# Kernel tuning notes

Hardware: AMD Instinct MI355X
Metric: run time of the kernel (lower is better)

The kernel has to match this reference:

```python
import jax, jax.numpy as jnp
import numpy as np

D_MODEL = 128
N_HEADS = 4
HEAD_DIM = D_MODEL // N_HEADS


def setup_inputs() -> dict:
    key = jax.random.key(0)
    ks = jax.random.split(key, 16)
    s = 0.05
    B, N, T = 1, 1024, 1024
    return {
        "node_states": jax.random.normal(ks[0], (B, N, D_MODEL), jnp.float32),
        "task_features": jax.random.normal(ks[1], (T, D_MODEL), jnp.float32),
        "in_proj_w": jax.random.normal(ks[2], (3 * D_MODEL, D_MODEL), jnp.float32) * s,
        "in_proj_b": jnp.zeros((3 * D_MODEL,), jnp.float32),
        "out_w": jax.random.normal(ks[3], (D_MODEL, D_MODEL), jnp.float32) * s,
        "out_b": jnp.zeros((D_MODEL,), jnp.float32),
        "W1": jax.random.normal(ks[4], (256, 256), jnp.float32) * s,
        "b1": jnp.zeros((256,), jnp.float32),
        "W2": jax.random.normal(ks[5], (128, 256), jnp.float32) * s,
        "b2": jnp.zeros((128,), jnp.float32),
        "W3": jax.random.normal(ks[6], (1, 128), jnp.float32) * s,
        "b3": jnp.zeros((1,), jnp.float32),
        "Wc1": jax.random.normal(ks[7], (256, D_MODEL), jnp.float32) * s,
        "bc1": jnp.zeros((256,), jnp.float32),
        "Wc2": jax.random.normal(ks[8], (32, 256), jnp.float32) * s,
        "bc2": jnp.zeros((32,), jnp.float32),
    }


def _mha(x, in_proj_w, in_proj_b, out_w, out_b):
    # x: [B, N, D]; torch nn.MultiheadAttention self-attention, batch_first.
    B, N, D = x.shape
    q = x @ in_proj_w[:D].T + in_proj_b[:D]
    k = x @ in_proj_w[D:2 * D].T + in_proj_b[D:2 * D]
    v = x @ in_proj_w[2 * D:].T + in_proj_b[2 * D:]
    def split(t):  # [B,N,D] -> [B,H,N,dh]
        return t.reshape(B, N, N_HEADS, HEAD_DIM).transpose(0, 2, 1, 3)
    qh, kh, vh = split(q), split(k), split(v)
    scores = jnp.einsum("bhqd,bhkd->bhqk", qh, kh) / jnp.sqrt(jnp.float32(HEAD_DIM))
    attn = jax.nn.softmax(scores, axis=-1)  # [B,H,N,N]
    ctx = jnp.einsum("bhqk,bhkd->bhqd", attn, vh)
    ctx = ctx.transpose(0, 2, 1, 3).reshape(B, N, D)
    out = ctx @ out_w.T + out_b
    attn_avg = attn.mean(axis=1)  # torch averages heads by default -> [B,N,N]
    return out, attn_avg


def reference(node_states, task_features, in_proj_w, in_proj_b, out_w, out_b,
              W1, b1, W2, b2, W3, b3, Wc1, bc1, Wc2, bc2):
    attended, attn_w = _mha(node_states, in_proj_w, in_proj_b, out_w, out_b)
    nodes = attended[0]  # original loop only uses batch 0: [N, D]
    # Linear on concat([task, node]) == split-weight sum; vectorize pairwise.
    t1 = task_features @ W1[:, :D_MODEL].T          # [T, 256]
    n1 = nodes @ W1[:, D_MODEL:].T                  # [N, 256]
    h1 = jax.nn.relu(t1[:, None, :] + n1[None, :, :] + b1)      # [T, N, 256]
    h2 = jax.nn.relu(jnp.einsum("tnc,kc->tnk", h1, W2) + b2)   # [T, N, 128]
    matching_scores = jax.nn.sigmoid(jnp.einsum("tnk,ok->tn", h2, W3) + b3[0])
    global_state = attended.mean(axis=1)            # [B, D]
    coordination_logits = jax.nn.relu(global_state @ Wc1.T + bc1) @ Wc2.T + bc2
    return matching_scores, coordination_logits, attn_w
```

## Files before the change

### kernel.cpp

```cpp
#include <hip/hip_runtime.h>
#include <hip/hip_fp16.h>
#include <stdint.h>


typedef __attribute__((ext_vector_type(4))) float floatx4;
typedef __attribute__((ext_vector_type(8))) _Float16 half8;

#define OFF_QKV  0x000000u
#define OFF_T1H  0x280000u
#define OFF_N1H  0x300000u
#define OFF_W2F  0x380000u
#define OFF_GS   0x398000u
#define OFF_SM   0x3A0000u
#define OFF_SL   0x3A8000u
#define OFF_SC   0x400000u
#define OFF_CTP  0xC00000u

__device__ __forceinline__ unsigned pkadd(unsigned a, unsigned b) {
    unsigned r; asm("v_pk_add_f16 %0, %1, %2" : "=v"(r) : "v"(a), "v"(b)); return r;
}
__device__ __forceinline__ unsigned pkmax(unsigned a, unsigned b) {
    unsigned r; asm("v_pk_max_f16 %0, %1, %2" : "=v"(r) : "v"(a), "v"(b)); return r;
}
__device__ __forceinline__ unsigned pk2h(float a, float b) {
    return (unsigned)__half_as_ushort(__float2half(a)) |
           ((unsigned)__half_as_ushort(__float2half(b)) << 16);
}
__device__ __forceinline__ float h2f(unsigned short u) {
    return __half2float(__ushort_as_half(u));
}

template<bool BIAS, bool F16OUT>
__device__ __forceinline__ void gemm_dev(
    const float* __restrict__ A, int lda,
    const float* __restrict__ B, int ldb,
    const float* __restrict__ bias,
    void* __restrict__ Cv, int ldc, int K, float scale,
    int m0, int n0, float (*As)[64], float (*Bs)[64])
{
    const int tid = threadIdx.x;
    const int tx = tid & 15, ty = tid >> 4;
    const int lr = tid >> 2;
    const int lk = (tid & 3) * 4;
    float c[4][4] = {};

    for (int k0 = 0; k0 < K; k0 += 16) {
        float4 a  = *(const float4*)&A[(long)(m0 + lr) * lda + k0 + lk];
        float4 bb = *(const float4*)&B[(long)(n0 + lr) * ldb + k0 + lk];
        __syncthreads();
        As[lk + 0][lr] = a.x;  As[lk + 1][lr] = a.y;  As[lk + 2][lr] = a.z;  As[lk + 3][lr] = a.w;
        Bs[lk + 0][lr] = bb.x; Bs[lk + 1][lr] = bb.y; Bs[lk + 2][lr] = bb.z; Bs[lk + 3][lr] = bb.w;
        __syncthreads();
#pragma unroll
        for (int k = 0; k < 16; k++) {
            float4 av = *(const float4*)&As[k][ty * 4];
            float4 bv = *(const float4*)&Bs[k][tx * 4];
            c[0][0] += av.x * bv.x; c[0][1] += av.x * bv.y; c[0][2] += av.x * bv.z; c[0][3] += av.x * bv.w;
            c[1][0] += av.y * bv.x; c[1][1] += av.y * bv.y; c[1][2] += av.y * bv.z; c[1][3] += av.y * bv.w;
            c[2][0] += av.z * bv.x; c[2][1] += av.z * bv.y; c[2][2] += av.z * bv.z; c[2][3] += av.z * bv.w;
            c[3][0] += av.w * bv.x; c[3][1] += av.w * bv.y; c[3][2] += av.w * bv.z; c[3][3] += av.w * bv.w;
        }
    }

    float bsv[4] = {0.f, 0.f, 0.f, 0.f};
    if (BIAS) {
        float4 t = *(const float4*)&bias[n0 + tx * 4];
        bsv[0] = t.x; bsv[1] = t.y; bsv[2] = t.z; bsv[3] = t.w;
    }
#pragma unroll
    for (int i = 0; i < 4; i++) {
        float v0 = c[i][0] * scale + bsv[0];
        float v1 = c[i][1] * scale + bsv[1];
        float v2 = c[i][2] * scale + bsv[2];
        float v3 = c[i][3] * scale + bsv[3];
        long m = m0 + ty * 4 + i;
        if (F16OUT) {
            unsigned short* Cp = (unsigned short*)Cv;
            ushort4 o;
            o.x = __half_as_ushort(__float2half(v0));
            o.y = __half_as_ushort(__float2half(v1));
            o.z = __half_as_ushort(__float2half(v2));
            o.w = __half_as_ushort(__float2half(v3));
            *(ushort4*)&Cp[m * ldc + n0 + tx * 4] = o;
        } else {
            float* Cp = (float*)Cv;
            *(float4*)&Cp[m * ldc + n0 + tx * 4] = make_float4(v0, v1, v2, v3);
        }
    }
}

__launch_bounds__(256)
__global__ void proj_fused(const float* __restrict__ node, const float* __restrict__ ipw,
                           const float* __restrict__ ipb,
                           const float* __restrict__ task, const float* __restrict__ W1,
                           const float* __restrict__ b1, const float* __restrict__ W2,
                           float* __restrict__ qkv, unsigned short* __restrict__ t1h,
                           unsigned short* __restrict__ w2f, float* __restrict__ gs)
{
    __shared__ float As[16][64], Bs[16][64];
    const int bid = blockIdx.x;
    if (bid < 96) {
        gemm_dev<true, false>(node, 128, ipw, 128, ipb, qkv, 384, 128, 1.0f,
                              (bid & 15) * 64, (bid >> 4) * 64, As, Bs);
    } else if (bid < 160) {
        const int b = bid - 96;
        gemm_dev<true, true>(task, 128, W1, 256, b1, t1h, 256, 128, 1.0f,
                             (b & 15) * 64, (b >> 4) * 64, As, Bs);
    } else if (bid < 176) {
        const int gtid = (bid - 160) * 256 + threadIdx.x;
        const int lane = gtid & 63, frag = gtid >> 6;
        const int cc = frag >> 3, ot = frag & 7;
        const float* src = &W2[(ot * 16 + (lane & 15)) * 256 + cc * 32 + (lane >> 4) * 8];
        uint4 o;
        o.x = pk2h(src[0], src[1]);
        o.y = pk2h(src[2], src[3]);
        o.z = pk2h(src[4], src[5]);
        o.w = pk2h(src[6], src[7]);
        ((uint4*)w2f)[gtid] = o;
    } else {
        if (threadIdx.x < 128) gs[threadIdx.x] = 0.f;
    }
}

__launch_bounds__(256)
__global__ void scores_kernel(const float* __restrict__ qkv, unsigned short* __restrict__ sc16)
{
    __shared__ float As[16][64], Bs[16][64];
    const int h = blockIdx.z;
    gemm_dev<false, true>(qkv + h * 32, 384, qkv + 128 + h * 32, 384, nullptr,
                          sc16 + ((size_t)h << 20), 1024, 32, 0.17677669529663687f,
                          blockIdx.x * 64, blockIdx.y * 64, As, Bs);
}

__launch_bounds__(256)
__global__ void attn_pre(const unsigned short* __restrict__ sc16,
                         float* __restrict__ sm, float* __restrict__ sl,
                         float* __restrict__ attn_out)
{
    __shared__ float Ps[4][1024];
    __shared__ float stm[4], stl[4];
    const int t = threadIdx.x;
    const int q = blockIdx.x;

#pragma unroll
    for (int h = 0; h < 4; h++) {
        ushort4 u = *(const ushort4*)&sc16[((size_t)h << 20) + (size_t)q * 1024 + t * 4];
        *(float4*)&Ps[h][t * 4] = make_float4(h2f(u.x), h2f(u.y), h2f(u.z), h2f(u.w));
    }
    __syncthreads();

    {
        const int h = t >> 6, ln = t & 63;
        float4 v[4];
        float mx = -1e30f;
#pragma unroll
        for (int i = 0; i < 4; i++) {
            v[i] = *(const float4*)&Ps[h][ln * 4 + i * 256];
            mx = fmaxf(mx, fmaxf(fmaxf(v[i].x, v[i].y), fmaxf(v[i].z, v[i].w)));
        }
#pragma unroll
        for (int m = 1; m < 64; m <<= 1) mx = fmaxf(mx, __shfl_xor(mx, m));
        float s = 0.f;
#pragma unroll
        for (int i = 0; i < 4; i++)
            s += __expf(v[i].x - mx) + __expf(v[i].y - mx) +
                 __expf(v[i].z - mx) + __expf(v[i].w - mx);
#pragma unroll
        for (int m = 1; m < 64; m <<= 1) s += __shfl_xor(s, m);
        if (ln == 0) {
            stm[h] = mx; stl[h] = s;
            sm[h * 1024 + q] = mx; sl[h * 1024 + q] = s;
        }
    }
    __syncthreads();

    float a0 = 0.f, a1 = 0.f, a2 = 0.f, a3 = 0.f;
#pragma unroll
    for (int h = 0; h < 4; h++) {
        const float m = stm[h], il = 1.0f / stl[h];
        float4 f = *(const float4*)&Ps[h][t * 4];
        a0 += __expf(f.x - m) * il;
        a1 += __expf(f.y - m) * il;
        a2 += __expf(f.z - m) * il;
        a3 += __expf(f.w - m) * il;
    }
    *(float4*)&attn_out[(size_t)q * 1024 + t * 4] =
        make_float4(0.25f * a0, 0.25f * a1, 0.25f * a2, 0.25f * a3);
}

__launch_bounds__(256)
__global__ void ctx_kernel(const unsigned short* __restrict__ sc16,
                           const float* __restrict__ sm, const float* __restrict__ sl,
                           const float* __restrict__ qkv, float* __restrict__ ctxp)
{
    const int h = blockIdx.z;
    const int q0 = blockIdx.x * 64;
    const int ks = blockIdx.y;
    const int kbase = ks * 128;
    __shared__ float As[32][64];
    __shared__ float Vs[32][32];
    const int tid = threadIdx.x;
    const int tx = tid & 15, ty = tid >> 4;
    const int sq = tid >> 3;
    const int sk4 = (tid & 7) * 4;
    float acc[4][2] = {};

    for (int k0 = kbase; k0 < kbase + 128; k0 += 32) {
        __syncthreads();
#pragma unroll
        for (int half = 0; half < 2; half++) {
            int q = sq + half * 32;
            float m = sm[h * 1024 + q0 + q];
            float il = 1.0f / sl[h * 1024 + q0 + q];
            ushort4 u = *(const ushort4*)&sc16[((size_t)h << 20) + (size_t)(q0 + q) * 1024 + k0 + sk4];
            As[sk4 + 0][q] = __expf(h2f(u.x) - m) * il;
            As[sk4 + 1][q] = __expf(h2f(u.y) - m) * il;
            As[sk4 + 2][q] = __expf(h2f(u.z) - m) * il;
            As[sk4 + 3][q] = __expf(h2f(u.w) - m) * il;
        }
        *(float4*)&Vs[sq][sk4] = *(const float4*)&qkv[(long)(k0 + sq) * 384 + 256 + h * 32 + sk4];
        __syncthreads();
#pragma unroll
        for (int k = 0; k < 32; k++) {
            float4 a = *(const float4*)&As[k][tx * 4];
            float b0 = Vs[k][ty * 2], b1 = Vs[k][ty * 2 + 1];
            acc[0][0] += a.x * b0; acc[0][1] += a.x * b1;
            acc[1][0] += a.y * b0; acc[1][1] += a.y * b1;
            acc[2][0] += a.z * b0; acc[2][1] += a.z * b1;
            acc[3][0] += a.w * b0; acc[3][1] += a.w * b1;
        }
    }
#pragma unroll
    for (int i = 0; i < 4; i++) {
        *(float2*)&ctxp[((size_t)ks * 1024 + (q0 + tx * 4 + i)) * 128 + h * 32 + ty * 2] =
            make_float2(acc[i][0], acc[i][1]);
    }
}

__launch_bounds__(256)
__global__ void attn_post(const float* __restrict__ ctxp, const float* __restrict__ outw,
                          const float* __restrict__ outb, const float* __restrict__ W1,
                          unsigned short* __restrict__ n1h, float* __restrict__ gs)
{
    __shared__ float ctxs[4][128];
    __shared__ float attr[4][128];
    const int t = threadIdx.x;
    const int q0 = blockIdx.x * 4;

#pragma unroll
    for (int s = 0; s < 2; s++) {
        const int idx = s * 256 + t;
        const int q = idx >> 7, d = idx & 127;
        float v = 0.f;
#pragma unroll
        for (int ks = 0; ks < 8; ks++)
            v += ctxp[((size_t)ks * 1024 + (q0 + q)) * 128 + d];
        ctxs[q][d] = v;
    }
    __syncthreads();

    {
        const int j = t & 127, qp = t >> 7;
        float a0 = outb[j], a1 = a0;
        const float* wr = &outw[j * 128];
        for (int d = 0; d < 128; d += 4) {
            float4 w  = *(const float4*)&wr[d];
            float4 c0 = *(const float4*)&ctxs[qp * 2 + 0][d];
            float4 c1 = *(const float4*)&ctxs[qp * 2 + 1][d];
            a0 += w.x * c0.x + w.y * c0.y + w.z * c0.z + w.w * c0.w;
            a1 += w.x * c1.x + w.y * c1.y + w.z * c1.z + w.w * c1.w;
        }
        attr[qp * 2 + 0][j] = a0;
        attr[qp * 2 + 1][j] = a1;
    }
    __syncthreads();
    if (t < 128) atomicAdd(&gs[t], attr[0][t] + attr[1][t] + attr[2][t] + attr[3][t]);

    {
        const int c = t;
        const float* wr = &W1[c * 256 + 128];
        float n[4] = {};
        for (int d = 0; d < 128; d += 4) {
            float4 w = *(const float4*)&wr[d];
#pragma unroll
            for (int q = 0; q < 4; q++) {
                float4 a = *(const float4*)&attr[q][d];
                n[q] += w.x * a.x + w.y * a.y + w.z * a.z + w.w * a.w;
            }
        }
#pragma unroll
        for (int q = 0; q < 4; q++)
            n1h[(size_t)(q0 + q) * 256 + c] = __half_as_ushort(__float2half(n[q]));
    }
}

__launch_bounds__(256, 2)
__global__ void score_kernel(const unsigned short* __restrict__ t1h,
                             const unsigned short* __restrict__ n1h,
                             const unsigned short* __restrict__ w2f,
                             const float* __restrict__ b2, const float* __restrict__ W3,
                             const float* __restrict__ b3, float* __restrict__ out,
                             const float* __restrict__ gs,
                             const float* __restrict__ Wc1, const float* __restrict__ bc1,
                             const float* __restrict__ Wc2, const float* __restrict__ bc2,
                             float* __restrict__ outc)
{
    __shared__ unsigned short w2s[32768];
    __shared__ float b2s[128], w3s[128];
    const int tid = threadIdx.x;

    if (blockIdx.y == 32) {
        if (blockIdx.x != 0) return;
        float* g  = (float*)w2s;
        float* hh = g + 128;
        if (tid < 128) g[tid] = gs[tid] * (1.0f / 1024.0f);
        __syncthreads();
        {
            float a = bc1[tid];
            const float* wr = &Wc1[tid * 128];
            for (int d = 0; d < 128; d += 4) {
                float4 w = *(const float4*)&wr[d];
                a += w.x * g[d] + w.y * g[d + 1] + w.z * g[d + 2] + w.w * g[d + 3];
            }
            hh[tid] = fmaxf(a, 0.f);
        }
        __syncthreads();
        if (tid < 32) {
            float a = bc2[tid];
            const float* wr = &Wc2[tid * 256];
            for (int c = 0; c < 256; c += 4) {
                float4 w = *(const float4*)&wr[c];
                a += w.x * hh[c] + w.y * hh[c + 1] + w.z * hh[c + 2] + w.w * hh[c + 3];
            }
            outc[tid] = a;
        }
        return;
    }

    const int lane = tid & 63;
    const int wv = tid >> 6;
    const int col = lane & 15;
    const int quad = lane >> 4;
    const int nb = blockIdx.x * 64 + wv * 16;
    const int tb = blockIdx.y * 32;

    {
        const uint4* src = (const uint4*)w2f;
        uint4* dst = (uint4*)w2s;
#pragma unroll
        for (int i = 0; i < 16; i++) dst[tid + i * 256] = src[tid + i * 256];
        if (tid < 128) { b2s[tid] = b2[tid]; w3s[tid] = W3[tid]; }
    }

    const int myn = nb + col;
    uint4 n1p[8];
#pragma unroll
    for (int cc = 0; cc < 8; cc++)
        n1p[cc] = *(const uint4*)(n1h + (size_t)myn * 256 + cc * 32 + quad * 8);

    const float b3s = b3[0];
    __syncthreads();

    for (int tg = 0; tg < 8; tg++) {
        floatx4 acc[4][8] = {};

#pragma unroll
        for (int cc = 0; cc < 8; cc++) {
            uint4 tp[4];
#pragma unroll
            for (int tt = 0; tt < 4; tt++)
                tp[tt] = *(const uint4*)(t1h + (size_t)(tb + tg * 4 + tt) * 256 + cc * 32 + quad * 8);

            const unsigned* npu = (const unsigned*)&n1p[cc];
            union { unsigned u[4]; half8 h; } af[4];
#pragma unroll
            for (int tt = 0; tt < 4; tt++) {
                const unsigned* tpu = (const unsigned*)&tp[tt];
#pragma unroll
                for (int p = 0; p < 4; p++)
                    af[tt].u[p] = pkmax(pkadd(tpu[p], npu[p]), 0u);
            }
#pragma unroll
            for (int ot = 0; ot < 8; ot++) {
                union { uint4 u; half8 h; } bf;
                bf.u = *(const uint4*)&w2s[((cc * 8 + ot) * 64 + lane) * 8];
#pragma unroll
                for (int tt = 0; tt < 4; tt++)
                    acc[tt][ot] = __builtin_amdgcn_mfma_f32_16x16x32_f16(bf.h, af[tt].h, acc[tt][ot], 0, 0, 0);
            }
        }

        float part[4] = {0.f, 0.f, 0.f, 0.f};
#pragma unroll
        for (int ot = 0; ot < 8; ot++) {
            float4 bq = *(const float4*)&b2s[ot * 16 + quad * 4];
            float4 wq = *(const float4*)&w3s[ot * 16 + quad * 4];
#pragma unroll
            for (int tt = 0; tt < 4; tt++) {
                floatx4 a = acc[tt][ot];
                part[tt] += fmaxf(a[0] + bq.x, 0.f) * wq.x + fmaxf(a[1] + bq.y, 0.f) * wq.y
                          + fmaxf(a[2] + bq.z, 0.f) * wq.z + fmaxf(a[3] + bq.w, 0.f) * wq.w;
            }
        }
        float outv = 0.f;
#pragma unroll
        for (int tt = 0; tt < 4; tt++) {
            float p = part[tt];
            p += __shfl_xor(p, 16);
            p += __shfl_xor(p, 32);
            if (quad == tt) outv = p;
        }
        out[(size_t)(tb + tg * 4 + quad) * 1024 + nb + col] =
            1.0f / (1.0f + __expf(-(outv + b3s)));
    }
}

extern "C" void kernel_launch(void* const* d_in, const int* in_sizes, int n_in,
                              void* d_out, int out_size, void* d_ws, size_t ws_size,
                              hipStream_t stream)
{
    const float* node = (const float*)d_in[0];
    const float* task = (const float*)d_in[1];
    const float* ipw  = (const float*)d_in[2];
    const float* ipb  = (const float*)d_in[3];
    const float* outw = (const float*)d_in[4];
    const float* outb = (const float*)d_in[5];
    const float* W1   = (const float*)d_in[6];
    const float* b1   = (const float*)d_in[7];
    const float* W2   = (const float*)d_in[8];
    const float* b2   = (const float*)d_in[9];
    const float* W3   = (const float*)d_in[10];
    const float* b3   = (const float*)d_in[11];
    const float* Wc1  = (const float*)d_in[12];
    const float* bc1  = (const float*)d_in[13];
    const float* Wc2  = (const float*)d_in[14];
    const float* bc2  = (const float*)d_in[15];

    char* ws = (char*)d_ws;
    float* qkv = (float*)(ws + OFF_QKV);
    unsigned short* t1h = (unsigned short*)(ws + OFF_T1H);
    unsigned short* n1h = (unsigned short*)(ws + OFF_N1H);
    unsigned short* w2f = (unsigned short*)(ws + OFF_W2F);
    float* gs = (float*)(ws + OFF_GS);
    float* sm = (float*)(ws + OFF_SM);
    float* sl = (float*)(ws + OFF_SL);
    unsigned short* sc16 = (unsigned short*)(ws + OFF_SC);
    float* ctxp = (float*)(ws + OFF_CTP);

    float* out_match = (float*)d_out;
    float* out_coord = out_match + 1048576;
    float* out_attn  = out_coord + 32;

    proj_fused<<<dim3(177, 1, 1), 256, 0, stream>>>(
        node, ipw, ipb, task, W1, b1, W2, qkv, t1h, w2f, gs);
    scores_kernel<<<dim3(16, 16, 4), 256, 0, stream>>>(qkv, sc16);
    attn_pre<<<dim3(1024, 1, 1), 256, 0, stream>>>(sc16, sm, sl, out_attn);
    ctx_kernel<<<dim3(16, 8, 4), 256, 0, stream>>>(sc16, sm, sl, qkv, ctxp);
    attn_post<<<dim3(256, 1, 1), 256, 0, stream>>>(ctxp, outw, outb, W1, n1h, gs);
    score_kernel<<<dim3(16, 33, 1), 256, 0, stream>>>(
        t1h, n1h, w2f, b2, W3, b3, out_match,
        gs, Wc1, bc1, Wc2, bc2, out_coord);
}
```

Before: 195.7 us.

## Restructure score kernel to 512-thread blocks with fewer task rows per wave

The pairwise scoring kernel now runs 8 waves per block over 128 nodes and 16 task rows, and each wave keeps 2 task rows instead of 4 live in its accumulators. Fewer accumulators lower register pressure, which allows more resident waves per CU to hide LDS and global latency. The layer-2 bias now seeds the accumulators instead of being added in the epilogue, and s_setprio brackets the MFMA block. In exchange, each t1h row and each LDS weight fragment feeds half as many MFMAs, so operand reuse per load drops, and half the lanes sit idle at the output store.

```diff
diff --git a/kernel.cpp b/kernel.cpp
--- a/kernel.cpp
+++ b/kernel.cpp
@@ -294,7 +294,7 @@
     }
 }
 
-__launch_bounds__(256, 2)
+__launch_bounds__(512, 4)
 __global__ void score_kernel(const unsigned short* __restrict__ t1h,
                              const unsigned short* __restrict__ n1h,
                              const unsigned short* __restrict__ w2f,
@@ -309,13 +309,13 @@
     __shared__ float b2s[128], w3s[128];
     const int tid = threadIdx.x;
 
-    if (blockIdx.y == 32) {
+    if (blockIdx.y == 64) {
         if (blockIdx.x != 0) return;
         float* g  = (float*)w2s;
         float* hh = g + 128;
         if (tid < 128) g[tid] = gs[tid] * (1.0f / 1024.0f);
         __syncthreads();
-        {
+        if (tid < 256) {
             float a = bc1[tid];
             const float* wr = &Wc1[tid * 128];
             for (int d = 0; d < 128; d += 4) {
@@ -341,14 +341,14 @@
     const int wv = tid >> 6;
     const int col = lane & 15;
     const int quad = lane >> 4;
-    const int nb = blockIdx.x * 64 + wv * 16;
-    const int tb = blockIdx.y * 32;
+    const int nb = blockIdx.x * 128 + wv * 16;
+    const int tb = blockIdx.y * 16;
 
     {
         const uint4* src = (const uint4*)w2f;
         uint4* dst = (uint4*)w2s;
 #pragma unroll
-        for (int i = 0; i < 16; i++) dst[tid + i * 256] = src[tid + i * 256];
+        for (int i = 0; i < 8; i++) dst[tid + i * 512] = src[tid + i * 512];
         if (tid < 128) { b2s[tid] = b2[tid]; w3s[tid] = W3[tid]; }
     }
 
@@ -359,59 +359,66 @@
         n1p[cc] = *(const uint4*)(n1h + (size_t)myn * 256 + cc * 32 + quad * 8);
 
     const float b3s = b3[0];
+    const unsigned short* tbase = t1h + (size_t)tb * 256 + quad * 8;
     __syncthreads();
 
     for (int tg = 0; tg < 8; tg++) {
-        floatx4 acc[4][8] = {};
+        floatx4 acc[2][8];
+#pragma unroll
+        for (int ot = 0; ot < 8; ot++) {
+            float4 bq = *(const float4*)&b2s[ot * 16 + quad * 4];
+            floatx4 bi = {bq.x, bq.y, bq.z, bq.w};
+            acc[0][ot] = bi;
+            acc[1][ot] = bi;
+        }
 
 #pragma unroll
         for (int cc = 0; cc < 8; cc++) {
-            uint4 tp[4];
-#pragma unroll
-            for (int tt = 0; tt < 4; tt++)
-                tp[tt] = *(const uint4*)(t1h + (size_t)(tb + tg * 4 + tt) * 256 + cc * 32 + quad * 8);
+            uint4 tp0 = *(const uint4*)(tbase + (size_t)(tg * 2 + 0) * 256 + cc * 32);
+            uint4 tp1 = *(const uint4*)(tbase + (size_t)(tg * 2 + 1) * 256 + cc * 32);
 
             const unsigned* npu = (const unsigned*)&n1p[cc];
-            union { unsigned u[4]; half8 h; } af[4];
-#pragma unroll
-            for (int tt = 0; tt < 4; tt++) {
-                const unsigned* tpu = (const unsigned*)&tp[tt];
-#pragma unroll
-                for (int p = 0; p < 4; p++)
-                    af[tt].u[p] = pkmax(pkadd(tpu[p], npu[p]), 0u);
-            }
+            const unsigned* t0u = (const unsigned*)&tp0;
+            const unsigned* t1u = (const unsigned*)&tp1;
+            union { unsigned u[4]; half8 h; } af[2];
+#pragma unroll
+            for (int p = 0; p < 4; p++) {
+                af[0].u[p] = pkmax(pkadd(t0u[p], npu[p]), 0u);
+                af[1].u[p] = pkmax(pkadd(t1u[p], npu[p]), 0u);
+            }
+            __builtin_amdgcn_s_setprio(1);
 #pragma unroll
             for (int ot = 0; ot < 8; ot++) {
                 union { uint4 u; half8 h; } bf;
                 bf.u = *(const uint4*)&w2s[((cc * 8 + ot) * 64 + lane) * 8];
-#pragma unroll
-                for (int tt = 0; tt < 4; tt++)
-                    acc[tt][ot] = __builtin_amdgcn_mfma_f32_16x16x32_f16(bf.h, af[tt].h, acc[tt][ot], 0, 0, 0);
-            }
-        }
-
-        float part[4] = {0.f, 0.f, 0.f, 0.f};
+                acc[0][ot] = __builtin_amdgcn_mfma_f32_16x16x32_f16(bf.h, af[0].h, acc[0][ot], 0, 0, 0);
+                acc[1][ot] = __builtin_amdgcn_mfma_f32_16x16x32_f16(bf.h, af[1].h, acc[1][ot], 0, 0, 0);
+            }
+            __builtin_amdgcn_s_setprio(0);
+        }
+
+        float part[2] = {0.f, 0.f};
 #pragma unroll
         for (int ot = 0; ot < 8; ot++) {
-            float4 bq = *(const float4*)&b2s[ot * 16 + quad * 4];
             float4 wq = *(const float4*)&w3s[ot * 16 + quad * 4];
 #pragma unroll
-            for (int tt = 0; tt < 4; tt++) {
+            for (int tt = 0; tt < 2; tt++) {
                 floatx4 a = acc[tt][ot];
-                part[tt] += fmaxf(a[0] + bq.x, 0.f) * wq.x + fmaxf(a[1] + bq.y, 0.f) * wq.y
-                          + fmaxf(a[2] + bq.z, 0.f) * wq.z + fmaxf(a[3] + bq.w, 0.f) * wq.w;
+                part[tt] += fmaxf(a[0], 0.f) * wq.x + fmaxf(a[1], 0.f) * wq.y
+                          + fmaxf(a[2], 0.f) * wq.z + fmaxf(a[3], 0.f) * wq.w;
             }
         }
         float outv = 0.f;
 #pragma unroll
-        for (int tt = 0; tt < 4; tt++) {
+        for (int tt = 0; tt < 2; tt++) {
             float p = part[tt];
             p += __shfl_xor(p, 16);
             p += __shfl_xor(p, 32);
             if (quad == tt) outv = p;
         }
-        out[(size_t)(tb + tg * 4 + quad) * 1024 + nb + col] =
-            1.0f / (1.0f + __expf(-(outv + b3s)));
+        if (quad < 2)
+            out[(size_t)(tb + tg * 2 + quad) * 1024 + nb + col] =
+                1.0f / (1.0f + __expf(-(outv + b3s)));
     }
 }
 
@@ -457,7 +464,7 @@
     attn_pre<<<dim3(1024, 1, 1), 256, 0, stream>>>(sc16, sm, sl, out_attn);
     ctx_kernel<<<dim3(16, 8, 4), 256, 0, stream>>>(sc16, sm, sl, qkv, ctxp);
     attn_post<<<dim3(256, 1, 1), 256, 0, stream>>>(ctxp, outw, outb, W1, n1h, gs);
-    score_kernel<<<dim3(16, 33, 1), 256, 0, stream>>>(
+    score_kernel<<<dim3(8, 65, 1), 512, 0, stream>>>(
         t1h, n1h, w2f, b2, W3, b3, out_match,
         gs, Wc1, bc1, Wc2, bc2, out_coord);
 }
```

Result: slower. 234.2 us (+19.6%).

## Split score-kernel output channels across wave pairs with shared-memory reduction

Applied to the files above, without the earlier changes.

Score kernel waves now split the 128 hidden output channels into two halves (oth) and each wave processes 8 task rows at a time over 16 nodes. Partial W3 dot products are combined across wave pairs through a double-buffered shared-memory array. The grid doubles along x so more blocks cover fewer nodes each. The b2 bias is folded into the accumulator initialisation, and s_setprio raises wave priority around the MFMA block. This is meant to improve MFMA issue density and parallelism. In exchange it adds a __syncthreads per pass, reloads n1 rows from global memory each pass, and doubles the per-block W2 copies into LDS across the grid.

```diff
diff --git a/kernel.cpp b/kernel.cpp
--- a/kernel.cpp
+++ b/kernel.cpp
@@ -307,6 +307,7 @@
 {
     __shared__ unsigned short w2s[32768];
     __shared__ float b2s[128], w3s[128];
+    __shared__ float red[2][2][8][16];
     const int tid = threadIdx.x;
 
     if (blockIdx.y == 32) {
@@ -341,8 +342,10 @@
     const int wv = tid >> 6;
     const int col = lane & 15;
     const int quad = lane >> 4;
-    const int nb = blockIdx.x * 64 + wv * 16;
-    const int tb = blockIdx.y * 32;
+    const int oth = wv & 1;
+    const int ng  = wv >> 1;
+    const int myn = blockIdx.x * 32 + ng * 16 + col;
+    const int tb  = blockIdx.y * 32;
 
     {
         const uint4* src = (const uint4*)w2f;
@@ -352,66 +355,77 @@
         if (tid < 128) { b2s[tid] = b2[tid]; w3s[tid] = W3[tid]; }
     }
 
-    const int myn = nb + col;
-    uint4 n1p[8];
-#pragma unroll
-    for (int cc = 0; cc < 8; cc++)
-        n1p[cc] = *(const uint4*)(n1h + (size_t)myn * 256 + cc * 32 + quad * 8);
-
+    const unsigned short* nbase = n1h + (size_t)myn * 256 + quad * 8;
+    const unsigned short* tbase = t1h + (size_t)tb * 256 + quad * 8;
     const float b3s = b3[0];
     __syncthreads();
 
-    for (int tg = 0; tg < 8; tg++) {
-        floatx4 acc[4][8] = {};
+    for (int p = 0; p < 4; p++) {
+        floatx4 acc[8][4];
+#pragma unroll
+        for (int otl = 0; otl < 4; otl++) {
+            float4 bq = *(const float4*)&b2s[(oth * 4 + otl) * 16 + quad * 4];
+            floatx4 bi = {bq.x, bq.y, bq.z, bq.w};
+#pragma unroll
+            for (int tt = 0; tt < 8; tt++) acc[tt][otl] = bi;
+        }
 
 #pragma unroll
         for (int cc = 0; cc < 8; cc++) {
-            uint4 tp[4];
-#pragma unroll
-            for (int tt = 0; tt < 4; tt++)
-                tp[tt] = *(const uint4*)(t1h + (size_t)(tb + tg * 4 + tt) * 256 + cc * 32 + quad * 8);
-
-            const unsigned* npu = (const unsigned*)&n1p[cc];
-            union { unsigned u[4]; half8 h; } af[4];
-#pragma unroll
-            for (int tt = 0; tt < 4; tt++) {
-                const unsigned* tpu = (const unsigned*)&tp[tt];
-#pragma unroll
-                for (int p = 0; p < 4; p++)
-                    af[tt].u[p] = pkmax(pkadd(tpu[p], npu[p]), 0u);
-            }
-#pragma unroll
-            for (int ot = 0; ot < 8; ot++) {
+            uint4 np = *(const uint4*)(nbase + cc * 32);
+            const unsigned* npu = (const unsigned*)&np;
+            union { unsigned u[4]; half8 h; } af[8];
+#pragma unroll
+            for (int tt = 0; tt < 8; tt++) {
+                uint4 tp = *(const uint4*)(tbase + (size_t)(p * 8 + tt) * 256 + cc * 32);
+                const unsigned* tpu = (const unsigned*)&tp;
+#pragma unroll
+                for (int q = 0; q < 4; q++)
+                    af[tt].u[q] = pkmax(pkadd(tpu[q], npu[q]), 0u);
+            }
+            __builtin_amdgcn_s_setprio(1);
+#pragma unroll
+            for (int otl = 0; otl < 4; otl++) {
                 union { uint4 u; half8 h; } bf;
-                bf.u = *(const uint4*)&w2s[((cc * 8 + ot) * 64 + lane) * 8];
-#pragma unroll
-                for (int tt = 0; tt < 4; tt++)
-                    acc[tt][ot] = __builtin_amdgcn_mfma_f32_16x16x32_f16(bf.h, af[tt].h, acc[tt][ot], 0, 0, 0);
-            }
-        }
-
-        float part[4] = {0.f, 0.f, 0.f, 0.f};
-#pragma unroll
-        for (int ot = 0; ot < 8; ot++) {
-            float4 bq = *(const float4*)&b2s[ot * 16 + quad * 4];
-            float4 wq = *(const float4*)&w3s[ot * 16 + quad * 4];
-#pragma unroll
-            for (int tt = 0; tt < 4; tt++) {
-                floatx4 a = acc[tt][ot];
-                part[tt] += fmaxf(a[0] + bq.x, 0.f) * wq.x + fmaxf(a[1] + bq.y, 0.f) * wq.y
-                          + fmaxf(a[2] + bq.z, 0.f) * wq.z + fmaxf(a[3] + bq.w, 0.f) * wq.w;
-            }
-        }
-        float outv = 0.f;
-#pragma unroll
-        for (int tt = 0; tt < 4; tt++) {
-            float p = part[tt];
-            p += __shfl_xor(p, 16);
-            p += __shfl_xor(p, 32);
-            if (quad == tt) outv = p;
-        }
-        out[(size_t)(tb + tg * 4 + quad) * 1024 + nb + col] =
-            1.0f / (1.0f + __expf(-(outv + b3s)));
+                bf.u = *(const uint4*)&w2s[((cc * 8 + oth * 4 + otl) * 64 + lane) * 8];
+#pragma unroll
+                for (int tt = 0; tt < 8; tt++)
+                    acc[tt][otl] = __builtin_amdgcn_mfma_f32_16x16x32_f16(bf.h, af[tt].h, acc[tt][otl], 0, 0, 0);
+            }
+            __builtin_amdgcn_s_setprio(0);
+        }
+
+        float part[8];
+#pragma unroll
+        for (int tt = 0; tt < 8; tt++) {
+            float s = 0.f;
+#pragma unroll
+            for (int otl = 0; otl < 4; otl++) {
+                float4 wq = *(const float4*)&w3s[(oth * 4 + otl) * 16 + quad * 4];
+                floatx4 a = acc[tt][otl];
+                s += fmaxf(a[0], 0.f) * wq.x + fmaxf(a[1], 0.f) * wq.y
+                   + fmaxf(a[2], 0.f) * wq.z + fmaxf(a[3], 0.f) * wq.w;
+            }
+            s += __shfl_xor(s, 16);
+            s += __shfl_xor(s, 32);
+            part[tt] = s;
+        }
+        const int pr = p & 1;
+        if (oth == 1) {
+#pragma unroll
+            for (int tt = 0; tt < 8; tt++)
+                if (quad == (tt & 3)) red[pr][ng][tt][col] = part[tt];
+        }
+        __syncthreads();
+        if (oth == 0) {
+#pragma unroll
+            for (int tt = 0; tt < 8; tt++)
+                if (quad == (tt & 3)) {
+                    float v = part[tt] + red[pr][ng][tt][col] + b3s;
+                    out[(size_t)(tb + p * 8 + tt) * 1024 + myn] =
+                        1.0f / (1.0f + __expf(-v));
+                }
+        }
     }
 }
 
@@ -457,7 +471,7 @@
     attn_pre<<<dim3(1024, 1, 1), 256, 0, stream>>>(sc16, sm, sl, out_attn);
     ctx_kernel<<<dim3(16, 8, 4), 256, 0, stream>>>(sc16, sm, sl, qkv, ctxp);
     attn_post<<<dim3(256, 1, 1), 256, 0, stream>>>(ctxp, outw, outb, W1, n1h, gs);
-    score_kernel<<<dim3(16, 33, 1), 256, 0, stream>>>(
+    score_kernel<<<dim3(32, 33, 1), 256, 0, stream>>>(
         t1h, n1h, w2f, b2, W3, b3, out_match,
         gs, Wc1, bc1, Wc2, bc2, out_coord);
 }
```

After: 203.6 us. 4.0% more time.
